# Kernel optimization log

Measured on AMD Instinct MI355X. Metric: run time of the kernel, lower is better.

The kernel has to match this reference:

```python
import jax, jax.numpy as jnp
import numpy as np
import math

EPS = 1e-5

def _ln(x, g, b):
    m = jnp.mean(x, axis=-1, keepdims=True)
    v = jnp.var(x, axis=-1, keepdims=True)
    return (x - m) * jax.lax.rsqrt(v + EPS) * g + b

def _rn_layer(x, W, g, b, A, Bb, Rw):
    # x: (B,S,in) -> (B,S,out). W: (out,in), A: (out,basis), Bb: (basis,out)
    S = x.shape[1]
    basis_dim = Bb.shape[0]
    n = _ln(x @ W.T, g, b)                      # (B,S,out)
    j = jnp.arange(S) % basis_dim               # (S,)
    Bv = Bb[j]                                  # (S,out)
    scal = jnp.einsum('bsd,sd->bs', n, Bv)      # (B,S)
    Av = A[:, j].T                              # (S,out)
    nf = scal[..., None] * Av                   # (B,S,out)
    res = x if Rw is None else x @ Rw.T
    return nf + res

def _ts_layer(x, M, g, b, P, Rw):
    # x: (B,S,in) -> (B,S,out). M: (out,in), P: (out,out,G)
    S = x.shape[1]
    D, _, G = P.shape
    t = _ln(x @ M.T, g, b)                      # (B,S,out)
    k = jnp.arange(S, dtype=jnp.float32)
    periods = (jnp.arange(D, dtype=jnp.float32)[:, None, None] * (D * G)
               + jnp.arange(D, dtype=jnp.float32)[None, :, None] * G
               + jnp.arange(G, dtype=jnp.float32)[None, None, :] + 2.0)  # (D,D,G)
    phi = jnp.cos(2.0 * math.pi * k[:, None, None, None] / periods)       # (S,D,D,G)
    # Nk[b,s,i] = sum_{j,g} P[i,j,g] * t[b,s,j] * phi[s,i,j,g]
    Wp = jnp.einsum('ijg,sijg->sij', P, phi)    # (S,D,D)
    Nk = jnp.einsum('sij,bsj->bsi', Wp, t)      # (B,S,D)
    return Nk + x @ Rw.T

def setup_inputs() -> dict:
    key = jax.random.key(0)
    ks = jax.random.split(key, 16)
    B, S = 2, 2048
    d0, d1, d2 = 512, 64, 512        # input_dim, ts out, final out
    bas1, G, bas3 = 64, 8, 64
    u = lambda k, sh, a: jax.random.uniform(k, sh, jnp.float32, -a, a)
    inp = {
        'x':  jax.random.normal(ks[0], (B, S, d0), jnp.float32),
        # Layer 1: RN 512->512 (in==out -> no residual proj)
        'W1': u(ks[1], (d0, d0), 0.1),
        'g1': jnp.ones((d0,), jnp.float32),
        'b1': jnp.zeros((d0,), jnp.float32),
        'A1': u(ks[2], (d0, bas1), 0.1),
        'B1': u(ks[3], (bas1, d0), 0.1),
        # Layer 2: TS 512->64
        'M2': u(ks[4], (d1, d0), 0.5),
        'g2': jnp.ones((d1,), jnp.float32),
        'b2': jnp.zeros((d1,), jnp.float32),
        'P2': u(ks[5], (d1, d1, G), 0.1),
        'R2': u(ks[6], (d1, d0), 0.1),
        # Layer 3: RN 64->512
        'W3': u(ks[7], (d2, d1), 0.1),
        'g3': jnp.ones((d2,), jnp.float32),
        'b3': jnp.zeros((d2,), jnp.float32),
        'A3': u(ks[8], (d2, bas3), 0.1),
        'B3': u(ks[9], (bas3, d2), 0.1),
        'R3': u(ks[10], (d2, d1), 0.1),
    }
    return inp

def reference(x, W1, g1, b1, A1, B1, M2, g2, b2, P2, R2, W3, g3, b3, A3, B3, R3):
    h = _rn_layer(x, W1, g1, b1, A1, B1, None)   # (B,S,512), identity residual
    h = _ts_layer(h, M2, g2, b2, P2, R2)         # (B,S,64)
    h = _rn_layer(h, W3, g3, b3, A3, B3, R3)     # (B,S,512)
    return h
```

## Files before the change

### kernel.cpp

```cpp
#include <hip/hip_runtime.h>
#include <math.h>

#define SEQ  2048
#define ROWS 4096
#define D0   512
#define D1   64

typedef short bf8 __attribute__((ext_vector_type(8)));
typedef float f4  __attribute__((ext_vector_type(4)));

__device__ __forceinline__ unsigned short f2bf(float f) {
    unsigned u = __float_as_uint(f);
    return (unsigned short)((u + 0x7fffu + ((u >> 16) & 1u)) >> 16);
}
__device__ __forceinline__ float bf2f(unsigned short u) {
    return __uint_as_float((unsigned)u << 16);
}
__device__ __forceinline__ void hilo(float f, unsigned short& h, unsigned short& l) {
    h = f2bf(f);
    float fh = bf2f(h);
    l = f2bf(f - fh);
}
__device__ __forceinline__ void cv4h(unsigned short* dh, int idx, float4 v) {
    ushort4 hv;
    hv.x = f2bf(v.x); hv.y = f2bf(v.y); hv.z = f2bf(v.z); hv.w = f2bf(v.w);
    *(ushort4*)(dh + idx) = hv;
}

__device__ __forceinline__ void async16(const void* g, void* l) {
    __builtin_amdgcn_global_load_lds(
        (const __attribute__((address_space(1))) unsigned int*)g,
        (__attribute__((address_space(3))) unsigned int*)l, 16, 0, 0);
}

__global__ __launch_bounds__(256) void convk(
        const float* __restrict__ x,  const float* __restrict__ W1,
        const float* __restrict__ M2, const float* __restrict__ R2,
        const float* __restrict__ W3, const float* __restrict__ R3,
        const float* __restrict__ A1, const float* __restrict__ A3,
        unsigned short* __restrict__ xh,
        unsigned short* __restrict__ W1h,
        unsigned short* __restrict__ C2h,
        unsigned short* __restrict__ C3h,
        float* __restrict__ A1T, float* __restrict__ A3T) {
    int c = blockIdx.x, tid = threadIdx.x;
    if (c < 1216) {
        const float* src; unsigned short* dh; int off;
        if      (c < 1024) { src = x;  dh = xh;          off = c; }
        else if (c < 1152) { src = W1; dh = W1h;         off = c - 1024; }
        else if (c < 1168) { src = M2; dh = C2h;         off = c - 1152; }
        else if (c < 1184) { src = R2; dh = C2h + 32768; off = c - 1168; }
        else if (c < 1200) { src = W3; dh = C3h;         off = c - 1184; }
        else               { src = R3; dh = C3h + 32768; off = c - 1200; }
        int base = off * 2048 + tid * 4;
        cv4h(dh, base,        *(const float4*)(src + base));
        cv4h(dh, base + 1024, *(const float4*)(src + base + 1024));
    } else {
        int gid = (c - 1216) * 256 + tid;
        int i = gid >> 6, j = gid & 63;
        A1T[j * 512 + i] = A1[gid];
        A3T[j * 512 + i] = A3[gid];
    }
}

template<bool ALO, int OM>
__global__ __launch_bounds__(256, 4) void gemm128t(
        const unsigned short* __restrict__ Ah, const unsigned short* __restrict__ Al,
        const unsigned short* __restrict__ Wh,
        float* __restrict__ Cf, unsigned short* __restrict__ Cb,
        int M, int N, int K, int Ks) {
    __shared__ __align__(16) unsigned short aH[8192];
    __shared__ __align__(16) unsigned short aL[ALO ? 8192 : 16];
    __shared__ __align__(16) unsigned short wH[4096];
    const int tid = threadIdx.x;
    const int wv  = tid >> 6;
    const int ln  = tid & 63;
    const int lm  = ln & 15;
    const int lq  = ln >> 4;
    const int bm  = blockIdx.y * 128;
    const int bn  = blockIdx.x * 64;
    const int k0  = blockIdx.z * Ks;

    f4 acc[2][4] = {};

    for (int kt = 0; kt < Ks; kt += 64) {
        const int kg = k0 + kt;
        __syncthreads();
#pragma unroll
        for (int i = 0; i < 4; ++i) {
            int slot = i * 256 + wv * 64 + ln;
            int row  = slot >> 3;
            int ch   = (slot & 7) ^ (row & 7);
            size_t go = (size_t)(bm + row) * K + kg + ch * 8;
            async16(Ah + go, aH + slot * 8);
            if constexpr (ALO) async16(Al + go, aL + slot * 8);
        }
#pragma unroll
        for (int i = 0; i < 2; ++i) {
            int slot = i * 256 + wv * 64 + ln;
            int row  = slot >> 3;
            int ch   = (slot & 7) ^ (row & 7);
            size_t go = (size_t)(bn + row) * K + kg + ch * 8;
            async16(Wh + go, wH + slot * 8);
        }
        __syncthreads();

#pragma unroll
        for (int kk = 0; kk < 2; ++kk) {
            const int ck = kk * 4 + lq;
            bf8 a_h[2], a_l[2], b_h[4];
#pragma unroll
            for (int t = 0; t < 2; ++t) {
                int r = wv * 32 + t * 16 + lm;
                a_h[t] = *(const bf8*)(aH + r * 64 + ((ck ^ (r & 7)) * 8));
                if constexpr (ALO)
                    a_l[t] = *(const bf8*)(aL + r * 64 + ((ck ^ (r & 7)) * 8));
            }
#pragma unroll
            for (int u = 0; u < 4; ++u) {
                int rb = u * 16 + lm;
                b_h[u] = *(const bf8*)(wH + rb * 64 + ((ck ^ (rb & 7)) * 8));
            }
#pragma unroll
            for (int t = 0; t < 2; ++t)
#pragma unroll
                for (int u = 0; u < 4; ++u) {
                    acc[t][u] = __builtin_amdgcn_mfma_f32_16x16x32_bf16(a_h[t], b_h[u], acc[t][u], 0, 0, 0);
                    if constexpr (ALO)
                        acc[t][u] = __builtin_amdgcn_mfma_f32_16x16x32_bf16(a_l[t], b_h[u], acc[t][u], 0, 0, 0);
                }
        }
    }

#pragma unroll
    for (int t = 0; t < 2; ++t)
#pragma unroll
        for (int u = 0; u < 4; ++u) {
            int row = bm + wv * 32 + t * 16 + lq * 4;
            int col = bn + u * 16 + lm;
#pragma unroll
            for (int r = 0; r < 4; ++r) {
                float v = acc[t][u][r];
                if constexpr (OM == 0) {
                    Cf[(size_t)blockIdx.z * M * N + (size_t)(row + r) * N + col] = v;
                } else if constexpr (OM == 1) {
                    Cb[(size_t)blockIdx.z * M * N + (size_t)(row + r) * N + col] = f2bf(v);
                } else {
                    if (col < 512) Cb[(size_t)(row + r) * 512 + col] = f2bf(v);
                    else           Cf[(size_t)(row + r) * 512 + col - 512] = v;
                }
            }
        }
}

__global__ __launch_bounds__(256) void lnrn(
        const unsigned short* __restrict__ Yb0,
        const unsigned short* __restrict__ Yb1,
        const float* __restrict__ RES,
        const float* __restrict__ g, const float* __restrict__ be,
        const float* __restrict__ Bb, const float* __restrict__ AaT,
        float* __restrict__ outf,
        unsigned short* __restrict__ outh, unsigned short* __restrict__ outl) {
    const int row = blockIdx.x * 4 + (threadIdx.x >> 6);
    const int l = threadIdx.x & 63;
    const int c = l * 8;
    ushort4 ua = *(const ushort4*)(Yb0 + (size_t)row * D0 + c);
    ushort4 ub = *(const ushort4*)(Yb0 + (size_t)row * D0 + c + 4);
    float4 y0, y1;
    y0.x = bf2f(ua.x); y0.y = bf2f(ua.y); y0.z = bf2f(ua.z); y0.w = bf2f(ua.w);
    y1.x = bf2f(ub.x); y1.y = bf2f(ub.y); y1.z = bf2f(ub.z); y1.w = bf2f(ub.w);
    if (Yb1) {
        ushort4 va = *(const ushort4*)(Yb1 + (size_t)row * D0 + c);
        ushort4 vb = *(const ushort4*)(Yb1 + (size_t)row * D0 + c + 4);
        y0.x += bf2f(va.x); y0.y += bf2f(va.y); y0.z += bf2f(va.z); y0.w += bf2f(va.w);
        y1.x += bf2f(vb.x); y1.y += bf2f(vb.y); y1.z += bf2f(vb.z); y1.w += bf2f(vb.w);
    }
    float sum = y0.x + y0.y + y0.z + y0.w + y1.x + y1.y + y1.z + y1.w;
    float ssq = y0.x*y0.x + y0.y*y0.y + y0.z*y0.z + y0.w*y0.w
              + y1.x*y1.x + y1.y*y1.y + y1.z*y1.z + y1.w*y1.w;
#pragma unroll
    for (int m = 1; m < 64; m <<= 1) {
        sum += __shfl_xor(sum, m, 64);
        ssq += __shfl_xor(ssq, m, 64);
    }
    float mean = sum * (1.0f / 512.0f);
    float var  = ssq * (1.0f / 512.0f) - mean * mean;
    float rstd = rsqrtf(var + 1e-5f);
    float4 g0 = *(const float4*)(g + c),  g1v = *(const float4*)(g + c + 4);
    float4 e0 = *(const float4*)(be + c), e1  = *(const float4*)(be + c + 4);
    float4 n0, n1;
    n0.x = (y0.x - mean) * rstd * g0.x  + e0.x;
    n0.y = (y0.y - mean) * rstd * g0.y  + e0.y;
    n0.z = (y0.z - mean) * rstd * g0.z  + e0.z;
    n0.w = (y0.w - mean) * rstd * g0.w  + e0.w;
    n1.x = (y1.x - mean) * rstd * g1v.x + e1.x;
    n1.y = (y1.y - mean) * rstd * g1v.y + e1.y;
    n1.z = (y1.z - mean) * rstd * g1v.z + e1.z;
    n1.w = (y1.w - mean) * rstd * g1v.w + e1.w;
    const int jm = row & 63;
    const float* bb = Bb + jm * D0 + c;
    float4 b0 = *(const float4*)bb, b1v = *(const float4*)(bb + 4);
    float p = n0.x*b0.x + n0.y*b0.y + n0.z*b0.z + n0.w*b0.w
            + n1.x*b1v.x + n1.y*b1v.y + n1.z*b1v.z + n1.w*b1v.w;
#pragma unroll
    for (int m = 1; m < 64; m <<= 1) p += __shfl_xor(p, m, 64);
    const float* av = AaT + jm * D0 + c;
    float4 a0 = *(const float4*)av, a1 = *(const float4*)(av + 4);
    const float* rs = RES + (size_t)row * D0 + c;
    float4 r0 = *(const float4*)rs, r1 = *(const float4*)(rs + 4);
    float4 v0, v1;
    v0.x = p*a0.x + r0.x; v0.y = p*a0.y + r0.y; v0.z = p*a0.z + r0.z; v0.w = p*a0.w + r0.w;
    v1.x = p*a1.x + r1.x; v1.y = p*a1.y + r1.y; v1.z = p*a1.z + r1.z; v1.w = p*a1.w + r1.w;
    if (outf) {
        *(float4*)(outf + (size_t)row * D0 + c)     = v0;
        *(float4*)(outf + (size_t)row * D0 + c + 4) = v1;
    } else {
        ushort4 h0, l0, h1, l1;
        hilo(v0.x, h0.x, l0.x); hilo(v0.y, h0.y, l0.y);
        hilo(v0.z, h0.z, l0.z); hilo(v0.w, h0.w, l0.w);
        hilo(v1.x, h1.x, l1.x); hilo(v1.y, h1.y, l1.y);
        hilo(v1.z, h1.z, l1.z); hilo(v1.w, h1.w, l1.w);
        *(ushort4*)(outh + (size_t)row * D0 + c)     = h0;
        *(ushort4*)(outl + (size_t)row * D0 + c)     = l0;
        *(ushort4*)(outh + (size_t)row * D0 + c + 4) = h1;
        *(ushort4*)(outl + (size_t)row * D0 + c + 4) = l1;
    }
}

#define C2S 524288
__global__ __launch_bounds__(256) void lnt(
        const float* __restrict__ C2, const float* __restrict__ g2,
        const float* __restrict__ b2,
        float* __restrict__ t, float* __restrict__ rsum) {
    const int r = blockIdx.x * 4 + (threadIdx.x >> 6);
    const int j = threadIdx.x & 63;
    size_t base = (size_t)r * 128 + j;
    float v = 0.f, rv = 0.f;
#pragma unroll
    for (int z = 0; z < 4; ++z) {
        v  += C2[(size_t)z * C2S + base];
        rv += C2[(size_t)z * C2S + base + 64];
    }
    float sum = v, ssq = v * v;
#pragma unroll
    for (int m = 1; m < 64; m <<= 1) {
        sum += __shfl_xor(sum, m, 64);
        ssq += __shfl_xor(ssq, m, 64);
    }
    float mean = sum * (1.0f / 64.0f);
    float var  = ssq * (1.0f / 64.0f) - mean * mean;
    float rstd = rsqrtf(var + 1e-5f);
    t[r * 64 + j]    = (v - mean) * rstd * g2[j] + b2[j];
    rsum[r * 64 + j] = rv;
}

__global__ __launch_bounds__(256) void tsk2(
        const float* __restrict__ t, const float* __restrict__ rsum,
        const float* __restrict__ P,
        unsigned short* __restrict__ Hh, unsigned short* __restrict__ Hl) {
    const int bid = blockIdx.x;
    const int i   = bid >> 3;
    const int sg  = bid & 7;
    const int w   = threadIdx.x >> 6;
    const int ln  = threadIdx.x & 63;
    const int s0  = sg * 256 + w * 64;
    const int idx = i * 64 + ln;
    const float* pp = P + idx * 8;
    const float sf0 = (float)s0;

    float k2c[8], ca[8], cb[8];
#pragma unroll
    for (int g = 0; g < 8; ++g) {
        float pf   = (float)(idx * 8 + g + 2);
        float invp = __builtin_amdgcn_rcpf(pf);
        k2c[g] = 2.0f * __builtin_amdgcn_cosf(invp);
        float q0 = floorf(sf0 * invp);
        float r0 = fmaf(-q0, pf, sf0);
        float f0 = r0 * invp; f0 -= floorf(f0);
        float c0 = __builtin_amdgcn_cosf(f0);
        float sf1 = sf0 + 1.0f;
        float q1 = floorf(sf1 * invp);
        float r1 = fmaf(-q1, pf, sf1);
        float f1 = r1 * invp; f1 -= floorf(f1);
        float c1 = __builtin_amdgcn_cosf(f1);
        float Pv = pp[g];
        ca[g] = Pv * c0;
        cb[g] = Pv * c1;
    }

    const int tb = s0 * 64 + ln;
    float t0c = t[tb], t1c = t[131072 + tb];
    float res0 = 0.f, res1 = 0.f;

    for (int st = 0; st < 64; st += 2) {
        float t0n  = t[tb + (st + 1) * 64];
        float t1n  = t[131072 + tb + (st + 1) * 64];
        float ws = ((ca[0] + ca[1]) + (ca[2] + ca[3]))
                 + ((ca[4] + ca[5]) + (ca[6] + ca[7]));
#pragma unroll
        for (int g = 0; g < 8; ++g) ca[g] = fmaf(k2c[g], cb[g], -ca[g]);
        float v0 = ws * t0c, v1 = ws * t1c;
#pragma unroll
        for (int m = 1; m < 64; m <<= 1) {
            v0 += __shfl_xor(v0, m, 64);
            v1 += __shfl_xor(v1, m, 64);
        }
        res0 = (ln == st) ? v0 : res0;
        res1 = (ln == st) ? v1 : res1;
        float t0n2 = t[tb + (st + 2) * 64];
        float t1n2 = t[131072 + tb + (st + 2) * 64];
        float ws2 = ((cb[0] + cb[1]) + (cb[2] + cb[3]))
                  + ((cb[4] + cb[5]) + (cb[6] + cb[7]));
#pragma unroll
        for (int g = 0; g < 8; ++g) cb[g] = fmaf(k2c[g], ca[g], -cb[g]);
        float v0b = ws2 * t0n, v1b = ws2 * t1n;
#pragma unroll
        for (int m = 1; m < 64; m <<= 1) {
            v0b += __shfl_xor(v0b, m, 64);
            v1b += __shfl_xor(v1b, m, 64);
        }
        res0 = (ln == st + 1) ? v0b : res0;
        res1 = (ln == st + 1) ? v1b : res1;
        t0c = t0n2; t1c = t1n2;
    }

    const int s = s0 + ln;
    {
        float v = res0 + rsum[(size_t)s * 64 + i];
        unsigned short h, l; hilo(v, h, l);
        Hh[(size_t)s * 64 + i] = h; Hl[(size_t)s * 64 + i] = l;
        float v1e = res1 + rsum[(size_t)(SEQ + s) * 64 + i];
        hilo(v1e, h, l);
        Hh[(size_t)(SEQ + s) * 64 + i] = h; Hl[(size_t)(SEQ + s) * 64 + i] = l;
    }
}

extern "C" void kernel_launch(void* const* d_in, const int* in_sizes, int n_in,
                              void* d_out, int out_size, void* d_ws, size_t ws_size,
                              hipStream_t stream) {
    const float* x  = (const float*)d_in[0];
    const float* W1 = (const float*)d_in[1];
    const float* g1 = (const float*)d_in[2];
    const float* b1 = (const float*)d_in[3];
    const float* A1 = (const float*)d_in[4];
    const float* B1 = (const float*)d_in[5];
    const float* M2 = (const float*)d_in[6];
    const float* g2 = (const float*)d_in[7];
    const float* b2 = (const float*)d_in[8];
    const float* P2 = (const float*)d_in[9];
    const float* R2 = (const float*)d_in[10];
    const float* W3 = (const float*)d_in[11];
    const float* g3 = (const float*)d_in[12];
    const float* b3 = (const float*)d_in[13];
    const float* A3 = (const float*)d_in[14];
    const float* B3 = (const float*)d_in[15];
    const float* R3 = (const float*)d_in[16];

    float* ws = (float*)d_ws;
    float* C2   = ws;
    float* C3r  = ws + 2097152;
    float* t    = ws + 4194304;
    float* rsum = ws + 4456448;
    float* A1T  = ws + 4718592;
    float* A3T  = ws + 4751360;
    unsigned short* us = (unsigned short*)(ws + 4784128);
    unsigned short* xh   = us;
    unsigned short* h1h  = us + 2097152;
    unsigned short* h1l  = us + 4194304;
    unsigned short* W1h  = us + 6291456;
    unsigned short* Wc2h = us + 6553600;
    unsigned short* Wc3h = us + 6619136;
    unsigned short* h2h  = us + 6684672;
    unsigned short* h2l  = us + 6946816;
    unsigned short* C1b  = us + 7208960;
    unsigned short* C3n  = us + 11403264;

    dim3 blk(256);

    convk<<<1344, blk, 0, stream>>>(x, W1, M2, R2, W3, R3, A1, A3,
                                    xh, W1h, Wc2h, Wc3h, A1T, A3T);

    gemm128t<false, 1><<<dim3(8, 32, 2), blk, 0, stream>>>(
        xh, xh, W1h, nullptr, C1b, ROWS, 512, 512, 256);
    lnrn<<<1024, blk, 0, stream>>>(C1b, C1b + (size_t)ROWS * 512, x,
                                   g1, b1, B1, A1T, nullptr, h1h, h1l);

    gemm128t<true, 0><<<dim3(2, 32, 4), blk, 0, stream>>>(
        h1h, h1l, Wc2h, C2, nullptr, ROWS, 128, 512, 128);
    lnt<<<1024, blk, 0, stream>>>(C2, g2, b2, t, rsum);
    tsk2<<<512, blk, 0, stream>>>(t, rsum, P2, h2h, h2l);

    gemm128t<true, 2><<<dim3(16, 32, 1), blk, 0, stream>>>(
        h2h, h2l, Wc3h, C3r, C3n, ROWS, 1024, 64, 64);
    lnrn<<<1024, blk, 0, stream>>>(C3n, nullptr, C3r, g3, b3, B3, A3T,
                                   (float*)d_out, nullptr, nullptr);
}
```

Baseline: 151.1 us.

## Fuse layer-1 and layer-3 GEMMs with LayerNorm/basis epilogues and convert x inline

Replaces the layer-1 GEMM plus separate LN/RN kernel with one kernel that converts x to bf16 on the fly, computes a 16-row by 512-column tile with MFMA, and runs the LayerNorm, basis projection and residual from shared memory. Layer 3 gets the same fusion, with the residual projection computed in the same tile. The layer-2 split-K partials are now stored as bf16 instead of fp32. This removes the x conversion pass, the intermediate bf16/fp32 round trips and two launches. In exchange, each 256-block grid reloads the full weight matrix per block, giving lower parallelism and repeated weight traffic. The bf16 partials also lose precision.

```diff
diff --git a/kernel.cpp b/kernel.cpp
--- a/kernel.cpp
+++ b/kernel.cpp
@@ -34,32 +34,145 @@
 }
 
 __global__ __launch_bounds__(256) void convk(
-        const float* __restrict__ x,  const float* __restrict__ W1,
-        const float* __restrict__ M2, const float* __restrict__ R2,
-        const float* __restrict__ W3, const float* __restrict__ R3,
-        const float* __restrict__ A1, const float* __restrict__ A3,
-        unsigned short* __restrict__ xh,
+        const float* __restrict__ W1, const float* __restrict__ M2,
+        const float* __restrict__ R2, const float* __restrict__ W3,
+        const float* __restrict__ R3, const float* __restrict__ A1,
+        const float* __restrict__ A3,
         unsigned short* __restrict__ W1h,
         unsigned short* __restrict__ C2h,
         unsigned short* __restrict__ C3h,
         float* __restrict__ A1T, float* __restrict__ A3T) {
     int c = blockIdx.x, tid = threadIdx.x;
-    if (c < 1216) {
+    if (c < 192) {
         const float* src; unsigned short* dh; int off;
-        if      (c < 1024) { src = x;  dh = xh;          off = c; }
-        else if (c < 1152) { src = W1; dh = W1h;         off = c - 1024; }
-        else if (c < 1168) { src = M2; dh = C2h;         off = c - 1152; }
-        else if (c < 1184) { src = R2; dh = C2h + 32768; off = c - 1168; }
-        else if (c < 1200) { src = W3; dh = C3h;         off = c - 1184; }
-        else               { src = R3; dh = C3h + 32768; off = c - 1200; }
+        if      (c < 128) { src = W1; dh = W1h;         off = c; }
+        else if (c < 144) { src = M2; dh = C2h;         off = c - 128; }
+        else if (c < 160) { src = R2; dh = C2h + 32768; off = c - 144; }
+        else if (c < 176) { src = W3; dh = C3h;         off = c - 160; }
+        else              { src = R3; dh = C3h + 32768; off = c - 176; }
         int base = off * 2048 + tid * 4;
         cv4h(dh, base,        *(const float4*)(src + base));
         cv4h(dh, base + 1024, *(const float4*)(src + base + 1024));
     } else {
-        int gid = (c - 1216) * 256 + tid;
-        int i = gid >> 6, j = gid & 63;
-        A1T[j * 512 + i] = A1[gid];
-        A3T[j * 512 + i] = A3[gid];
+        int g0 = ((c - 192) * 256 + tid) * 2;
+#pragma unroll
+        for (int e = g0; e < g0 + 2; ++e) {
+            int i = e >> 6, j = e & 63;
+            A1T[j * 512 + i] = A1[e];
+            A3T[j * 512 + i] = A3[e];
+        }
+    }
+}
+
+__global__ __launch_bounds__(256) void g1f(
+        const float* __restrict__ x, const unsigned short* __restrict__ W1h,
+        const float* __restrict__ g1, const float* __restrict__ b1,
+        const float* __restrict__ B1, const float* __restrict__ A1T,
+        unsigned short* __restrict__ h1h, unsigned short* __restrict__ h1l) {
+    __shared__ __align__(16) unsigned short smem[32768];
+    unsigned short* wS = smem;
+    float (*cS)[516] = (float(*)[516])smem;
+    const int tid = threadIdx.x;
+    const int w   = tid >> 6;
+    const int ln  = tid & 63;
+    const int lm  = ln & 15;
+    const int lq  = ln >> 4;
+    const int bm  = blockIdx.x * 16;
+
+    f4 acc[8] = {};
+
+    for (int kt = 0; kt < 8; ++kt) {
+        __syncthreads();
+        bf8 af[2];
+#pragma unroll
+        for (int kk = 0; kk < 2; ++kk) {
+            const float* xp = x + (size_t)(bm + lm) * 512 + kt * 64 + kk * 32 + lq * 8;
+            float4 u0 = *(const float4*)xp;
+            float4 u1 = *(const float4*)(xp + 4);
+            bf8 a;
+            a[0] = (short)f2bf(u0.x); a[1] = (short)f2bf(u0.y);
+            a[2] = (short)f2bf(u0.z); a[3] = (short)f2bf(u0.w);
+            a[4] = (short)f2bf(u1.x); a[5] = (short)f2bf(u1.y);
+            a[6] = (short)f2bf(u1.z); a[7] = (short)f2bf(u1.w);
+            af[kk] = a;
+        }
+#pragma unroll
+        for (int i = 0; i < 16; ++i) {
+            int slot = i * 256 + tid;
+            int row  = slot >> 3;
+            int cg   = (slot & 7) ^ (row & 7);
+            async16(W1h + (size_t)row * 512 + kt * 64 + cg * 8, wS + slot * 8);
+        }
+        __syncthreads();
+#pragma unroll
+        for (int it = 0; it < 8; ++it) {
+#pragma unroll
+            for (int kk = 0; kk < 2; ++kk) {
+                int rb = w * 128 + it * 16 + lm;
+                bf8 bh = *(const bf8*)(wS + rb * 64 + (((kk * 4 + lq) ^ (rb & 7)) * 8));
+                acc[it] = __builtin_amdgcn_mfma_f32_16x16x32_bf16(af[kk], bh, acc[it], 0, 0, 0);
+            }
+        }
+    }
+    __syncthreads();
+#pragma unroll
+    for (int it = 0; it < 8; ++it)
+#pragma unroll
+        for (int r = 0; r < 4; ++r)
+            cS[lq * 4 + r][w * 128 + it * 16 + lm] = acc[it][r];
+    __syncthreads();
+
+    for (int q = 0; q < 4; ++q) {
+        const int row = w * 4 + q;
+        const int gr  = bm + row;
+        const int c   = ln * 8;
+        float4 y0 = *(const float4*)&cS[row][c];
+        float4 y1 = *(const float4*)&cS[row][c + 4];
+        float sum = y0.x + y0.y + y0.z + y0.w + y1.x + y1.y + y1.z + y1.w;
+        float ssq = y0.x*y0.x + y0.y*y0.y + y0.z*y0.z + y0.w*y0.w
+                  + y1.x*y1.x + y1.y*y1.y + y1.z*y1.z + y1.w*y1.w;
+#pragma unroll
+        for (int m = 1; m < 64; m <<= 1) {
+            sum += __shfl_xor(sum, m, 64);
+            ssq += __shfl_xor(ssq, m, 64);
+        }
+        float mean = sum * (1.0f / 512.0f);
+        float var  = ssq * (1.0f / 512.0f) - mean * mean;
+        float rstd = rsqrtf(var + 1e-5f);
+        float4 g0 = *(const float4*)(g1 + c), g1v = *(const float4*)(g1 + c + 4);
+        float4 e0 = *(const float4*)(b1 + c), e1  = *(const float4*)(b1 + c + 4);
+        float4 n0, n1;
+        n0.x = (y0.x - mean) * rstd * g0.x  + e0.x;
+        n0.y = (y0.y - mean) * rstd * g0.y  + e0.y;
+        n0.z = (y0.z - mean) * rstd * g0.z  + e0.z;
+        n0.w = (y0.w - mean) * rstd * g0.w  + e0.w;
+        n1.x = (y1.x - mean) * rstd * g1v.x + e1.x;
+        n1.y = (y1.y - mean) * rstd * g1v.y + e1.y;
+        n1.z = (y1.z - mean) * rstd * g1v.z + e1.z;
+        n1.w = (y1.w - mean) * rstd * g1v.w + e1.w;
+        const int jm = gr & 63;
+        const float* bb = B1 + jm * D0 + c;
+        float4 b0 = *(const float4*)bb, b1v = *(const float4*)(bb + 4);
+        float p = n0.x*b0.x + n0.y*b0.y + n0.z*b0.z + n0.w*b0.w
+                + n1.x*b1v.x + n1.y*b1v.y + n1.z*b1v.z + n1.w*b1v.w;
+#pragma unroll
+        for (int m = 1; m < 64; m <<= 1) p += __shfl_xor(p, m, 64);
+        const float* av = A1T + jm * D0 + c;
+        float4 a0 = *(const float4*)av, a1 = *(const float4*)(av + 4);
+        const float* rs = x + (size_t)gr * D0 + c;
+        float4 r0 = *(const float4*)rs, r1 = *(const float4*)(rs + 4);
+        float4 v0, v1;
+        v0.x = p*a0.x + r0.x; v0.y = p*a0.y + r0.y; v0.z = p*a0.z + r0.z; v0.w = p*a0.w + r0.w;
+        v1.x = p*a1.x + r1.x; v1.y = p*a1.y + r1.y; v1.z = p*a1.z + r1.z; v1.w = p*a1.w + r1.w;
+        ushort4 h0, l0, h1v, l1;
+        hilo(v0.x, h0.x, l0.x); hilo(v0.y, h0.y, l0.y);
+        hilo(v0.z, h0.z, l0.z); hilo(v0.w, h0.w, l0.w);
+        hilo(v1.x, h1v.x, l1.x); hilo(v1.y, h1v.y, l1.y);
+        hilo(v1.z, h1v.z, l1.z); hilo(v1.w, h1v.w, l1.w);
+        *(ushort4*)(h1h + (size_t)gr * D0 + c)     = h0;
+        *(ushort4*)(h1l + (size_t)gr * D0 + c)     = l0;
+        *(ushort4*)(h1h + (size_t)gr * D0 + c + 4) = h1v;
+        *(ushort4*)(h1l + (size_t)gr * D0 + c + 4) = l1;
     }
 }
 
@@ -141,95 +254,17 @@
 #pragma unroll
             for (int r = 0; r < 4; ++r) {
                 float v = acc[t][u][r];
-                if constexpr (OM == 0) {
+                if constexpr (OM == 0)
                     Cf[(size_t)blockIdx.z * M * N + (size_t)(row + r) * N + col] = v;
-                } else if constexpr (OM == 1) {
+                else
                     Cb[(size_t)blockIdx.z * M * N + (size_t)(row + r) * N + col] = f2bf(v);
-                } else {
-                    if (col < 512) Cb[(size_t)(row + r) * 512 + col] = f2bf(v);
-                    else           Cf[(size_t)(row + r) * 512 + col - 512] = v;
-                }
             }
         }
-}
-
-__global__ __launch_bounds__(256) void lnrn(
-        const unsigned short* __restrict__ Yb0,
-        const unsigned short* __restrict__ Yb1,
-        const float* __restrict__ RES,
-        const float* __restrict__ g, const float* __restrict__ be,
-        const float* __restrict__ Bb, const float* __restrict__ AaT,
-        float* __restrict__ outf,
-        unsigned short* __restrict__ outh, unsigned short* __restrict__ outl) {
-    const int row = blockIdx.x * 4 + (threadIdx.x >> 6);
-    const int l = threadIdx.x & 63;
-    const int c = l * 8;
-    ushort4 ua = *(const ushort4*)(Yb0 + (size_t)row * D0 + c);
-    ushort4 ub = *(const ushort4*)(Yb0 + (size_t)row * D0 + c + 4);
-    float4 y0, y1;
-    y0.x = bf2f(ua.x); y0.y = bf2f(ua.y); y0.z = bf2f(ua.z); y0.w = bf2f(ua.w);
-    y1.x = bf2f(ub.x); y1.y = bf2f(ub.y); y1.z = bf2f(ub.z); y1.w = bf2f(ub.w);
-    if (Yb1) {
-        ushort4 va = *(const ushort4*)(Yb1 + (size_t)row * D0 + c);
-        ushort4 vb = *(const ushort4*)(Yb1 + (size_t)row * D0 + c + 4);
-        y0.x += bf2f(va.x); y0.y += bf2f(va.y); y0.z += bf2f(va.z); y0.w += bf2f(va.w);
-        y1.x += bf2f(vb.x); y1.y += bf2f(vb.y); y1.z += bf2f(vb.z); y1.w += bf2f(vb.w);
-    }
-    float sum = y0.x + y0.y + y0.z + y0.w + y1.x + y1.y + y1.z + y1.w;
-    float ssq = y0.x*y0.x + y0.y*y0.y + y0.z*y0.z + y0.w*y0.w
-              + y1.x*y1.x + y1.y*y1.y + y1.z*y1.z + y1.w*y1.w;
-#pragma unroll
-    for (int m = 1; m < 64; m <<= 1) {
-        sum += __shfl_xor(sum, m, 64);
-        ssq += __shfl_xor(ssq, m, 64);
-    }
-    float mean = sum * (1.0f / 512.0f);
-    float var  = ssq * (1.0f / 512.0f) - mean * mean;
-    float rstd = rsqrtf(var + 1e-5f);
-    float4 g0 = *(const float4*)(g + c),  g1v = *(const float4*)(g + c + 4);
-    float4 e0 = *(const float4*)(be + c), e1  = *(const float4*)(be + c + 4);
-    float4 n0, n1;
-    n0.x = (y0.x - mean) * rstd * g0.x  + e0.x;
-    n0.y = (y0.y - mean) * rstd * g0.y  + e0.y;
-    n0.z = (y0.z - mean) * rstd * g0.z  + e0.z;
-    n0.w = (y0.w - mean) * rstd * g0.w  + e0.w;
-    n1.x = (y1.x - mean) * rstd * g1v.x + e1.x;
-    n1.y = (y1.y - mean) * rstd * g1v.y + e1.y;
-    n1.z = (y1.z - mean) * rstd * g1v.z + e1.z;
-    n1.w = (y1.w - mean) * rstd * g1v.w + e1.w;
-    const int jm = row & 63;
-    const float* bb = Bb + jm * D0 + c;
-    float4 b0 = *(const float4*)bb, b1v = *(const float4*)(bb + 4);
-    float p = n0.x*b0.x + n0.y*b0.y + n0.z*b0.z + n0.w*b0.w
-            + n1.x*b1v.x + n1.y*b1v.y + n1.z*b1v.z + n1.w*b1v.w;
-#pragma unroll
-    for (int m = 1; m < 64; m <<= 1) p += __shfl_xor(p, m, 64);
-    const float* av = AaT + jm * D0 + c;
-    float4 a0 = *(const float4*)av, a1 = *(const float4*)(av + 4);
-    const float* rs = RES + (size_t)row * D0 + c;
-    float4 r0 = *(const float4*)rs, r1 = *(const float4*)(rs + 4);
-    float4 v0, v1;
-    v0.x = p*a0.x + r0.x; v0.y = p*a0.y + r0.y; v0.z = p*a0.z + r0.z; v0.w = p*a0.w + r0.w;
-    v1.x = p*a1.x + r1.x; v1.y = p*a1.y + r1.y; v1.z = p*a1.z + r1.z; v1.w = p*a1.w + r1.w;
-    if (outf) {
-        *(float4*)(outf + (size_t)row * D0 + c)     = v0;
-        *(float4*)(outf + (size_t)row * D0 + c + 4) = v1;
-    } else {
-        ushort4 h0, l0, h1, l1;
-        hilo(v0.x, h0.x, l0.x); hilo(v0.y, h0.y, l0.y);
-        hilo(v0.z, h0.z, l0.z); hilo(v0.w, h0.w, l0.w);
-        hilo(v1.x, h1.x, l1.x); hilo(v1.y, h1.y, l1.y);
-        hilo(v1.z, h1.z, l1.z); hilo(v1.w, h1.w, l1.w);
-        *(ushort4*)(outh + (size_t)row * D0 + c)     = h0;
-        *(ushort4*)(outl + (size_t)row * D0 + c)     = l0;
-        *(ushort4*)(outh + (size_t)row * D0 + c + 4) = h1;
-        *(ushort4*)(outl + (size_t)row * D0 + c + 4) = l1;
-    }
 }
 
 #define C2S 524288
 __global__ __launch_bounds__(256) void lnt(
-        const float* __restrict__ C2, const float* __restrict__ g2,
+        const unsigned short* __restrict__ C2b, const float* __restrict__ g2,
         const float* __restrict__ b2,
         float* __restrict__ t, float* __restrict__ rsum) {
     const int r = blockIdx.x * 4 + (threadIdx.x >> 6);
@@ -238,8 +273,8 @@
     float v = 0.f, rv = 0.f;
 #pragma unroll
     for (int z = 0; z < 4; ++z) {
-        v  += C2[(size_t)z * C2S + base];
-        rv += C2[(size_t)z * C2S + base + 64];
+        v  += bf2f(C2b[(size_t)z * C2S + base]);
+        rv += bf2f(C2b[(size_t)z * C2S + base + 64]);
     }
     float sum = v, ssq = v * v;
 #pragma unroll
@@ -332,6 +367,112 @@
         float v1e = res1 + rsum[(size_t)(SEQ + s) * 64 + i];
         hilo(v1e, h, l);
         Hh[(size_t)(SEQ + s) * 64 + i] = h; Hl[(size_t)(SEQ + s) * 64 + i] = l;
+    }
+}
+
+__global__ __launch_bounds__(256) void g3f(
+        const unsigned short* __restrict__ h2h, const unsigned short* __restrict__ h2l,
+        const unsigned short* __restrict__ Wc3h,
+        const float* __restrict__ g3, const float* __restrict__ b3,
+        const float* __restrict__ B3, const float* __restrict__ A3T,
+        float* __restrict__ out) {
+    __shared__ __align__(16) unsigned short smem[32768];
+    unsigned short* wS = smem;
+    float (*cS)[1024] = (float(*)[1024])smem;
+    const int tid = threadIdx.x;
+    const int w   = tid >> 6;
+    const int ln  = tid & 63;
+    const int lm  = ln & 15;
+    const int lq  = ln >> 4;
+    const int bm  = blockIdx.x * 16;
+
+    bf8 ah[2], al[2];
+#pragma unroll
+    for (int kk = 0; kk < 2; ++kk) {
+        size_t ao = (size_t)(bm + lm) * 64 + kk * 32 + lq * 8;
+        ah[kk] = *(const bf8*)(h2h + ao);
+        al[kk] = *(const bf8*)(h2l + ao);
+    }
+
+    f4 acc[2][8] = {};
+
+#pragma unroll
+    for (int ch = 0; ch < 2; ++ch) {
+        __syncthreads();
+#pragma unroll
+        for (int i = 0; i < 16; ++i) {
+            int slot = i * 256 + tid;
+            int row  = slot >> 3;
+            int cg   = (slot & 7) ^ (row & 7);
+            async16(Wc3h + (size_t)(ch * 512 + row) * 64 + cg * 8, wS + slot * 8);
+        }
+        __syncthreads();
+#pragma unroll
+        for (int it = 0; it < 8; ++it) {
+#pragma unroll
+            for (int kk = 0; kk < 2; ++kk) {
+                int rb = w * 128 + it * 16 + lm;
+                bf8 bh = *(const bf8*)(wS + rb * 64 + (((kk * 4 + lq) ^ (rb & 7)) * 8));
+                acc[ch][it] = __builtin_amdgcn_mfma_f32_16x16x32_bf16(ah[kk], bh, acc[ch][it], 0, 0, 0);
+                acc[ch][it] = __builtin_amdgcn_mfma_f32_16x16x32_bf16(al[kk], bh, acc[ch][it], 0, 0, 0);
+            }
+        }
+    }
+    __syncthreads();
+#pragma unroll
+    for (int ch = 0; ch < 2; ++ch)
+#pragma unroll
+        for (int it = 0; it < 8; ++it)
+#pragma unroll
+            for (int r = 0; r < 4; ++r)
+                cS[lq * 4 + r][ch * 512 + w * 128 + it * 16 + lm] = acc[ch][it][r];
+    __syncthreads();
+
+    for (int q = 0; q < 4; ++q) {
+        const int row = w * 4 + q;
+        const int gr  = bm + row;
+        const int c   = ln * 8;
+        float4 y0 = *(const float4*)&cS[row][c];
+        float4 y1 = *(const float4*)&cS[row][c + 4];
+        float sum = y0.x + y0.y + y0.z + y0.w + y1.x + y1.y + y1.z + y1.w;
+        float ssq = y0.x*y0.x + y0.y*y0.y + y0.z*y0.z + y0.w*y0.w
+                  + y1.x*y1.x + y1.y*y1.y + y1.z*y1.z + y1.w*y1.w;
+#pragma unroll
+        for (int m = 1; m < 64; m <<= 1) {
+            sum += __shfl_xor(sum, m, 64);
+            ssq += __shfl_xor(ssq, m, 64);
+        }
+        float mean = sum * (1.0f / 512.0f);
+        float var  = ssq * (1.0f / 512.0f) - mean * mean;
+        float rstd = rsqrtf(var + 1e-5f);
+        float4 g0 = *(const float4*)(g3 + c), g1v = *(const float4*)(g3 + c + 4);
+        float4 e0 = *(const float4*)(b3 + c), e1  = *(const float4*)(b3 + c + 4);
+        float4 n0, n1;
+        n0.x = (y0.x - mean) * rstd * g0.x  + e0.x;
+        n0.y = (y0.y - mean) * rstd * g0.y  + e0.y;
+        n0.z = (y0.z - mean) * rstd * g0.z  + e0.z;
+        n0.w = (y0.w - mean) * rstd * g0.w  + e0.w;
+        n1.x = (y1.x - mean) * rstd * g1v.x + e1.x;
+        n1.y = (y1.y - mean) * rstd * g1v.y + e1.y;
+        n1.z = (y1.z - mean) * rstd * g1v.z + e1.z;
+        n1.w = (y1.w - mean) * rstd * g1v.w + e1.w;
+        const int jm = gr & 63;
+        const float* bb = B3 + jm * D0 + c;
+        float4 b0 = *(const float4*)bb, b1v = *(const float4*)(bb + 4);
+        float p = n0.x*b0.x + n0.y*b0.y + n0.z*b0.z + n0.w*b0.w
+                + n1.x*b1v.x + n1.y*b1v.y + n1.z*b1v.z + n1.w*b1v.w;
+#pragma unroll
+        for (int m = 1; m < 64; m <<= 1) p += __shfl_xor(p, m, 64);
+        const float* av = A3T + jm * D0 + c;
+        float4 a0 = *(const float4*)av, a1 = *(const float4*)(av + 4);
+        float4 r0, r1;
+        r0 = *(const float4*)&cS[row][512 + c];
+        r1 = *(const float4*)&cS[row][512 + c + 4];
+        float4 v0, v1;
+        v0.x = p*a0.x + r0.x; v0.y = p*a0.y + r0.y; v0.z = p*a0.z + r0.z; v0.w = p*a0.w + r0.w;
+        v1.x = p*a1.x + r1.x; v1.y = p*a1.y + r1.y; v1.z = p*a1.z + r1.z; v1.w = p*a1.w + r1.w;
+        *(float4*)(out + (size_t)gr * D0 + c)     = v0;
+        *(float4*)(out + (size_t)gr * D0 + c + 4) = v1;
     }
 }
 
@@ -357,41 +498,32 @@
     const float* R3 = (const float*)d_in[16];
 
     float* ws = (float*)d_ws;
-    float* C2   = ws;
-    float* C3r  = ws + 2097152;
-    float* t    = ws + 4194304;
-    float* rsum = ws + 4456448;
-    float* A1T  = ws + 4718592;
-    float* A3T  = ws + 4751360;
-    unsigned short* us = (unsigned short*)(ws + 4784128);
-    unsigned short* xh   = us;
-    unsigned short* h1h  = us + 2097152;
-    unsigned short* h1l  = us + 4194304;
-    unsigned short* W1h  = us + 6291456;
-    unsigned short* Wc2h = us + 6553600;
-    unsigned short* Wc3h = us + 6619136;
-    unsigned short* h2h  = us + 6684672;
-    unsigned short* h2l  = us + 6946816;
-    unsigned short* C1b  = us + 7208960;
-    unsigned short* C3n  = us + 11403264;
+    float* t    = ws;
+    float* rsum = ws + 262144;
+    float* A1T  = ws + 524288;
+    float* A3T  = ws + 557056;
+    unsigned short* us = (unsigned short*)(ws + 589824);
+    unsigned short* h1h  = us;
+    unsigned short* h1l  = us + 2097152;
+    unsigned short* W1h  = us + 4194304;
+    unsigned short* Wc2h = us + 4456448;
+    unsigned short* Wc3h = us + 4521984;
+    unsigned short* h2h  = us + 4587520;
+    unsigned short* h2l  = us + 4849664;
+    unsigned short* C2b  = us + 5111808;
 
     dim3 blk(256);
 
-    convk<<<1344, blk, 0, stream>>>(x, W1, M2, R2, W3, R3, A1, A3,
-                                    xh, W1h, Wc2h, Wc3h, A1T, A3T);
-
-    gemm128t<false, 1><<<dim3(8, 32, 2), blk, 0, stream>>>(
-        xh, xh, W1h, nullptr, C1b, ROWS, 512, 512, 256);
-    lnrn<<<1024, blk, 0, stream>>>(C1b, C1b + (size_t)ROWS * 512, x,
-                                   g1, b1, B1, A1T, nullptr, h1h, h1l);
-
-    gemm128t<true, 0><<<dim3(2, 32, 4), blk, 0, stream>>>(
-        h1h, h1l, Wc2h, C2, nullptr, ROWS, 128, 512, 128);
-    lnt<<<1024, blk, 0, stream>>>(C2, g2, b2, t, rsum);
+    convk<<<256, blk, 0, stream>>>(W1, M2, R2, W3, R3, A1, A3,
+                                   W1h, Wc2h, Wc3h, A1T, A3T);
+
+    g1f<<<256, blk, 0, stream>>>(x, W1h, g1, b1, B1, A1T, h1h, h1l);
+
+    gemm128t<true, 1><<<dim3(2, 32, 4), blk, 0, stream>>>(
+        h1h, h1l, Wc2h, nullptr, C2b, ROWS, 128, 512, 128);
+    lnt<<<1024, blk, 0, stream>>>(C2b, g2, b2, t, rsum);
     tsk2<<<512, blk, 0, stream>>>(t, rsum, P2, h2h, h2l);
 
-    gemm128t<true, 2><<<dim3(16, 32, 1), blk, 0, stream>>>(
-        h2h, h2l, Wc3h, C3r, C3n, ROWS, 1024, 64, 64);
-    lnrn<<<1024, blk, 0, stream>>>(C3n, nullptr, C3r, g3, b3, B3, A3T,
-                                   (float*)d_out, nullptr, nullptr);
-}
+    g3f<<<256, blk, 0, stream>>>(h2h, h2l, Wc3h, g3, b3, B3, A3T,
+                                 (float*)d_out);
+}
```

Result: no change. 153.0 us (+1.3%).
